# Kernel optimization log

Hardware: AMD Instinct MI355X
Metric: run time of the kernel (lower is better)

Reference implementation:

```python
import jax, jax.numpy as jnp
import numpy as np

ANCHOR_SIZE = np.array([[32.64, 47.68], [50.24, 108.16], [126.72, 96.32], [78.4, 201.92], [178.24, 178.56], [129.6, 294.72], [331.84, 194.56], [227.84, 325.76], [365.44, 358.72]], dtype=np.float32).reshape(3, 3, 2)
STRIDES = [8, 16, 32]
INPUT_SIZE = 640
A = 3            # anchors per level
C = 80           # num_classes
CONF_T = 0.3
NMS_T = 0.5
TOPK = 1000      # fixed candidate budget for jit-compatible greedy NMS
CLS_OFFSET = 4.0 # boxes are in [0,1]; offsetting by class id makes cross-class IoU ~0


def _make_grids():
    gs, ss, aw = [], [], []
    for i, s in enumerate(STRIDES):
        hs = ws = INPUT_SIZE // s
        yy, xx = np.meshgrid(np.arange(hs), np.arange(ws), indexing='ij')
        gs.append(np.stack([xx, yy], -1).reshape(hs * ws, 1, 2).astype(np.float32))
        ss.append(np.full((hs * ws, A, 2), s, np.float32))
        aw.append(np.tile(ANCHOR_SIZE[i][None], (hs * ws, 1, 1)))
    return (jnp.asarray(np.concatenate(gs, 0)),   # [HW, 1, 2]
            jnp.asarray(np.concatenate(ss, 0)),   # [HW, A, 2]
            jnp.asarray(np.concatenate(aw, 0)))   # [HW, A, 2]

GRID, STRIDE_T, ANCH_WH = _make_grids()


def _conv(x, w, b, pad):
    y = jax.lax.conv_general_dilated(x, w, (1, 1), pad, dimension_numbers=('NCHW', 'OIHW', 'NCHW'))
    return y + b[None, :, None, None]


def _conv_bn_lrelu(x, w, b, g, be, m, v):
    y = _conv(x, w, b, 'SAME')
    y = (y - m[None, :, None, None]) * (g / jnp.sqrt(v + 1e-5))[None, :, None, None] + be[None, :, None, None]
    return jnp.where(y > 0, y, 0.1 * y)  # LeakyReLU(0.1)


def _split_head(pred):
    # pred: [B, A*(1+C+4), H, W] -> conf [B,HW*A,1], cls [B,HW*A,C], txt [B,HW,A,4]
    B, ch, H, W = pred.shape
    p = pred.transpose(0, 2, 3, 1).reshape(B, H * W, ch)
    conf = p[:, :, :A].reshape(B, H * W * A, 1)
    cls = p[:, :, A:(1 + C) * A].reshape(B, H * W * A, C)
    txt = p[:, :, (1 + C) * A:].reshape(B, H * W, A, 4)
    return conf, cls, txt


def _nms_single(boxes, sc, cls):
    # boxes [N,4] in [0,1], sc [N], cls [N] -> keep mask [N]
    N = boxes.shape[0]
    masked = jnp.where(sc >= CONF_T, sc, -1.0)
    vals, idx = jax.lax.top_k(masked, TOPK)           # sorted desc, like argsort()[::-1]
    valid = vals >= CONF_T
    b = boxes[idx] + cls[idx].astype(boxes.dtype)[:, None] * CLS_OFFSET
    x1, y1, x2, y2 = b[:, 0], b[:, 1], b[:, 2], b[:, 3]
    area = (x2 - x1) * (y2 - y1)
    xx1 = jnp.maximum(x1[:, None], x1[None, :])
    yy1 = jnp.maximum(y1[:, None], y1[None, :])
    xx2 = jnp.minimum(x2[:, None], x2[None, :])
    yy2 = jnp.minimum(y2[:, None], y2[None, :])
    inter = jnp.maximum(1e-28, xx2 - xx1) * jnp.maximum(1e-28, yy2 - yy1)
    iou = inter / (area[:, None] + area[None, :] - inter)
    sup = iou > NMS_T
    rng = jnp.arange(TOPK)

    def body(i, keep):
        suppressed = jnp.any(keep & sup[:, i] & (rng < i))
        return keep.at[i].set(valid[i] & ~suppressed)

    keep_c = jax.lax.fori_loop(0, TOPK, body, jnp.zeros(TOPK, dtype=bool))
    return jnp.zeros(N, dtype=bool).at[idx].set(keep_c)


def _forward_dense(p3, p4, p5, w1, b1, g1, be1, m1, v1, pw1, pb1, w2, b2, g2, be2, m2, v2, pw2, pb2, w3, b3, g3, be3, m3, v3, pw3, pb3):
    pred_1 = _conv(_conv_bn_lrelu(p3, w1, b1, g1, be1, m1, v1), pw1, pb1, 'VALID')
    pred_2 = _conv(_conv_bn_lrelu(p4, w2, b2, g2, be2, m2, v2), pw2, pb2, 'VALID')
    pred_3 = _conv(_conv_bn_lrelu(p5, w3, b3, g3, be3, m3, v3), pw3, pb3, 'VALID')
    confs, clss, txts = zip(*[_split_head(p) for p in (pred_1, pred_2, pred_3)])
    conf = jnp.concatenate(confs, 1)   # [B, N, 1]
    cls = jnp.concatenate(clss, 1)     # [B, N, C]
    txt = jnp.concatenate(txts, 1)     # [B, HW, A, 4]
    B = txt.shape[0]
    # decode_boxes
    cxy = (jax.nn.sigmoid(txt[..., :2]) + GRID[None]) * STRIDE_T[None]
    wh = jnp.exp(txt[..., 2:]) * ANCH_WH[None]
    xywh = jnp.concatenate([cxy, wh], -1).reshape(B, -1, 4)
    x1y1 = xywh[..., :2] - xywh[..., 2:] / 2
    x2y2 = xywh[..., :2] + xywh[..., 2:] / 2
    boxes = jnp.clip(jnp.concatenate([x1y1, x2y2], -1) / INPUT_SIZE, 0.0, 1.0)  # [B,N,4]
    scores = jax.nn.softmax(cls, axis=-1) * jax.nn.sigmoid(conf)                 # [B,N,C]
    cls_inds = jnp.argmax(scores, axis=-1)                                        # [B,N]
    sc = jnp.max(scores, axis=-1)                                                 # [B,N]
    cx = (boxes[..., 0] + boxes[..., 2]) / 2 * INPUT_SIZE
    cy = (boxes[..., 1] + boxes[..., 3]) / 2 * INPUT_SIZE
    bw = (boxes[..., 2] - boxes[..., 0]) * INPUT_SIZE
    bh = (boxes[..., 3] - boxes[..., 1]) * INPUT_SIZE
    dets5 = jnp.stack([cx, cy, bw, bh, sc], -1)  # [B,N,5]
    return dets5, boxes, sc, cls_inds


def setup_inputs() -> dict:
    key = jax.random.key(0)
    ks = iter(jax.random.split(key, 64))
    d = {
        'p3': jax.random.normal(next(ks), (8, 128, 80, 80), jnp.float32),
        'p4': jax.random.normal(next(ks), (8, 256, 40, 40), jnp.float32),
        'p5': jax.random.normal(next(ks), (8, 512, 20, 20), jnp.float32),
    }
    for lvl, (cin, cout) in zip('123', [(128, 256), (256, 512), (512, 1024)]):
        fan = cin * 9
        d['w' + lvl] = jax.random.normal(next(ks), (cout, cin, 3, 3), jnp.float32) * fan ** -0.5
        d['b' + lvl] = jax.random.normal(next(ks), (cout,), jnp.float32) * 0.1
        d['g' + lvl] = jax.random.uniform(next(ks), (cout,), jnp.float32) * 0.5 + 0.75
        d['be' + lvl] = jax.random.normal(next(ks), (cout,), jnp.float32) * 0.1
        d['m' + lvl] = jax.random.normal(next(ks), (cout,), jnp.float32) * 0.1
        d['v' + lvl] = jax.random.uniform(next(ks), (cout,), jnp.float32) * 0.5 + 0.5
        abC = A * (1 + 4 + C)
        d['pw' + lvl] = jax.random.normal(next(ks), (abC, cout, 1, 1), jnp.float32) * cout ** -0.5
        d['pb' + lvl] = jax.random.normal(next(ks), (abC,), jnp.float32) * 0.1
    return d


def reference(p3, p4, p5, w1, b1, g1, be1, m1, v1, pw1, pb1, w2, b2, g2, be2, m2, v2, pw2, pb2, w3, b3, g3, be3, m3, v3, pw3, pb3):
    dets5, boxes, sc, cls_inds = _forward_dense(p3, p4, p5, w1, b1, g1, be1, m1, v1, pw1, pb1, w2, b2, g2, be2, m2, v2, pw2, pb2, w3, b3, g3, be3, m3, v3, pw3, pb3)
    keep = jax.vmap(_nms_single)(boxes, sc, cls_inds)  # [B,N] bool, per-class greedy NMS
    return dets5, cls_inds.astype(jnp.int32), keep
```

## Files before the change

kernel.cpp:

```cpp
#include <hip/hip_runtime.h>
#include <hip/hip_bf16.h>
#include <stdint.h>
#include <math.h>

typedef unsigned long long ull;
typedef __attribute__((ext_vector_type(8))) _Float16 f16x8;
typedef __attribute__((ext_vector_type(4))) float f32x4;

__device__ __forceinline__ void f16_split(float v, short& hi, short& lo) {
  _Float16 h = (_Float16)v;
  float r = v - (float)h;
  _Float16 l = (_Float16)(r * 2048.f);
  hi = __builtin_bit_cast(short, h);
  lo = __builtin_bit_cast(short, l);
}
__device__ __forceinline__ unsigned pk2(short a, short b) {
  return (unsigned)(unsigned short)a | ((unsigned)(unsigned short)b << 16);
}

__global__ __launch_bounds__(256)
void xprep(const float* __restrict__ x, short* __restrict__ XC, int HW, int CIN) {
  __shared__ float T[32 * 132];
  const int p0 = blockIdx.x * 128, c0 = blockIdx.y * 32, b = blockIdx.z;
  const int tid = threadIdx.x;
#pragma unroll
  for (int i = 0; i < 16; ++i) {
    int u = tid + i * 256;
    int ch = u >> 7, px = u & 127;
    int gp = p0 + px;
    float v = 0.f;
    if (gp < HW) v = x[((size_t)b * CIN + c0 + ch) * HW + gp];
    T[ch * 132 + px] = v;
  }
  __syncthreads();
  const int px = tid & 127, half = tid >> 7;
  const int gp = p0 + px;
  if (gp < HW) {
    short h[16], l[16];
#pragma unroll
    for (int k = 0; k < 16; ++k)
      f16_split(T[(half * 16 + k) * 132 + px], h[k], l[k]);
    short* dh = XC + ((size_t)b * HW + gp) * 2 * CIN + c0 + half * 16;
    short* dl = dh + CIN;
    int4 a, bq;
    a.x = pk2(h[0], h[1]); a.y = pk2(h[2], h[3]); a.z = pk2(h[4], h[5]); a.w = pk2(h[6], h[7]);
    bq.x = pk2(h[8], h[9]); bq.y = pk2(h[10], h[11]); bq.z = pk2(h[12], h[13]); bq.w = pk2(h[14], h[15]);
    *(int4*)dh = a; *(int4*)(dh + 8) = bq;
    a.x = pk2(l[0], l[1]); a.y = pk2(l[2], l[3]); a.z = pk2(l[4], l[5]); a.w = pk2(l[6], l[7]);
    bq.x = pk2(l[8], l[9]); bq.y = pk2(l[10], l[11]); bq.z = pk2(l[12], l[13]); bq.w = pk2(l[14], l[15]);
    *(int4*)dl = a; *(int4*)(dl + 8) = bq;
  }
}

__global__ __launch_bounds__(256)
void wprep(const float* __restrict__ w, const float* __restrict__ g,
           const float* __restrict__ v, short* __restrict__ WF, int CIN, int lgNOG) {
  const int NOG = 1 << lgNOG;
  int e = blockIdx.x * 256 + threadIdx.x;
  int lane = e & 63;
  int og = (e >> 6) & (NOG - 1);
  int r = e >> (6 + lgNOG);
  int t = r % 9, kc = r / 9;
  int oc = og * 16 + (lane & 15);
  int icb = kc * 32 + (lane >> 4) * 8;
  float s = g[oc] / sqrtf(v[oc] + 1e-5f);
  short h[8], l[8];
#pragma unroll
  for (int j = 0; j < 8; ++j) {
    float val = w[((size_t)oc * CIN + icb + j) * 9 + t] * s;
    f16_split(val, h[j], l[j]);
  }
  size_t base = ((size_t)(kc * 9 + t) * NOG + og) * 1024 + lane * 8;
  int4 a;
  a.x = pk2(h[0], h[1]); a.y = pk2(h[2], h[3]); a.z = pk2(h[4], h[5]); a.w = pk2(h[6], h[7]);
  *(int4*)&WF[base] = a;
  a.x = pk2(l[0], l[1]); a.y = pk2(l[2], l[3]); a.z = pk2(l[4], l[5]); a.w = pk2(l[6], l[7]);
  *(int4*)&WF[base + 512] = a;
}

__global__ __launch_bounds__(256)
void hwprep(const float* __restrict__ pw, short* __restrict__ WH, int CIN) {
  int e = blockIdx.x * 256 + threadIdx.x;
  int lane = e & 63;
  int og = (e >> 6) & 15;
  int kc = e >> 10;
  int oc = og * 16 + (lane & 15);
  int ic0 = kc * 32 + (lane >> 4) * 8;
  short h[8], l[8];
#pragma unroll
  for (int j = 0; j < 8; ++j) {
    float val = (oc < 255) ? pw[(size_t)oc * CIN + ic0 + j] : 0.f;
    f16_split(val, h[j], l[j]);
  }
  size_t base = ((size_t)(kc * 16 + og) * 2) * 512 + lane * 8;
  int4 a;
  a.x = pk2(h[0], h[1]); a.y = pk2(h[2], h[3]); a.z = pk2(h[4], h[5]); a.w = pk2(h[6], h[7]);
  *(int4*)&WH[base] = a;
  a.x = pk2(l[0], l[1]); a.y = pk2(l[2], l[3]); a.z = pk2(l[4], l[5]); a.w = pk2(l[6], l[7]);
  *(int4*)&WH[base + 512] = a;
}

__global__ __launch_bounds__(256)
void bfold(const float* __restrict__ b, const float* __restrict__ g,
           const float* __restrict__ be, const float* __restrict__ m,
           const float* __restrict__ v, float* __restrict__ bias2, int n) {
  int i = blockIdx.x * 256 + threadIdx.x;
  if (i < n) bias2[i] = (b[i] - m[i]) * (g[i] / sqrtf(v[i] + 1e-5f)) + be[i];
}

template<int CIN, int COUT, int H, int W, int ROWS, int OG>
__global__ __launch_bounds__(256, 2)
void conv3x3_mfma(const short* __restrict__ XC, const short* __restrict__ WF,
                  const float* __restrict__ bias2, short* __restrict__ ACT) {
  constexpr int HW = H * W, WP = W + 2, NROW = ROWS + 2, NOGT = COUT / 16;
  constexpr int BSH = OG * 1024;
  __shared__ short Xs[NROW * WP * 64];
  __shared__ short Bs[2][BSH];
  const int tid = threadIdx.x, lane = tid & 63, wave = tid >> 6;
  const int tile = blockIdx.x, octile = blockIdx.y, b = blockIdx.z;
  const int r0 = tile * ROWS;
  const int tile_px0 = r0 * W;
  const int kgrp = lane >> 4, lm = lane & 15;
  int Pbase[5];
#pragma unroll
  for (int m = 0; m < 5; ++m) {
    int pl = wave * 80 + m * 16 + lm;
    Pbase[m] = (pl / W) * WP + (pl % W);
  }
  f32x4 acc0[5][OG], acc1[5][OG];
#pragma unroll
  for (int m = 0; m < 5; ++m)
#pragma unroll
    for (int og = 0; og < OG; ++og) {
      acc0[m][og] = (f32x4){0.f, 0.f, 0.f, 0.f};
      acc1[m][og] = (f32x4){0.f, 0.f, 0.f, 0.f};
    }

  const size_t xcb = (size_t)b * HW * 2 * CIN;
  const int og0 = octile * OG;

  for (int u = tid; u < NROW * 2 * 8; u += 256) {
    int sub = u & 7, rc = u >> 3;
    int pxi = (rc >> 1) * WP + ((rc & 1) ? (W + 1) : 0);
    *(int4*)&Xs[pxi * 64 + ((sub ^ (pxi & 7)) << 3)] = make_int4(0, 0, 0, 0);
  }

  for (int kc = 0; kc < CIN / 32; ++kc) {
    for (int g0 = tid; g0 < NROW * W * 8; g0 += 256) {
      int sub = g0 & 7, px = g0 >> 3;
      int rr = px / W, col = px % W;
      int gr = r0 - 1 + rr;
      int pxi = rr * WP + col + 1;
      int dst = pxi * 64 + ((sub ^ (pxi & 7)) << 3);
      if (gr >= 0 && gr < H) {
        const short* src = XC + xcb + (size_t)(gr * W + col) * 2 * CIN +
                           ((sub & 4) ? CIN : 0) + kc * 32 + (sub & 3) * 8;
        *(int4*)&Xs[dst] = *(const int4*)src;
      } else {
        *(int4*)&Xs[dst] = make_int4(0, 0, 0, 0);
      }
    }
    {
      const short* src = WF + ((size_t)(kc * 9 + 0) * NOGT + og0) * 1024 + tid * (BSH / 256);
      *(int4*)&Bs[0][tid * (BSH / 256)] = *(const int4*)src;
      if constexpr (OG == 4)
        *(int4*)&Bs[0][tid * 16 + 8] = *(const int4*)(src + 8);
    }
    __syncthreads();
#pragma unroll 1
    for (int t = 0; t < 9; ++t) {
      int4 r0v, r1v;
      if (t < 8) {
        const short* src = WF + ((size_t)(kc * 9 + t + 1) * NOGT + og0) * 1024 + tid * (BSH / 256);
        r0v = *(const int4*)src;
        if constexpr (OG == 4) r1v = *(const int4*)(src + 8);
      }
      const short* bs = Bs[t & 1];
      f16x8 bh[OG], bl[OG];
#pragma unroll
      for (int og = 0; og < OG; ++og) {
        bh[og] = *(const f16x8*)&bs[(og * 2 + 0) * 512 + lane * 8];
        bl[og] = *(const f16x8*)&bs[(og * 2 + 1) * 512 + lane * 8];
      }
      const int tp = (t / 3) * WP + (t % 3);
#pragma unroll
      for (int m = 0; m < 5; ++m) {
        int P = Pbase[m] + tp;
        int base = P * 64, ph = P & 7;
        f16x8 ah = *(const f16x8*)&Xs[base + ((kgrp ^ ph) << 3)];
        f16x8 al = *(const f16x8*)&Xs[base + (((kgrp + 4) ^ ph) << 3)];
#pragma unroll
        for (int og = 0; og < OG; ++og) {
          acc0[m][og] = __builtin_amdgcn_mfma_f32_16x16x32_f16(bh[og], ah, acc0[m][og], 0, 0, 0);
          acc1[m][og] = __builtin_amdgcn_mfma_f32_16x16x32_f16(bl[og], ah, acc1[m][og], 0, 0, 0);
          acc1[m][og] = __builtin_amdgcn_mfma_f32_16x16x32_f16(bh[og], al, acc1[m][og], 0, 0, 0);
        }
      }
      if (t < 8) {
        *(int4*)&Bs[(t + 1) & 1][tid * (BSH / 256)] = r0v;
        if constexpr (OG == 4)
          *(int4*)&Bs[(t + 1) & 1][tid * 16 + 8] = r1v;
      }
      __syncthreads();
    }
  }
#pragma unroll
  for (int og = 0; og < OG; ++og) {
    const int oc0 = octile * OG * 16 + og * 16 + kgrp * 4;
    float4 bv = *(const float4*)&bias2[oc0];
#pragma unroll
    for (int m = 0; m < 5; ++m) {
      int px = tile_px0 + wave * 80 + m * 16 + lm;
      if (px < HW) {
        f32x4 v0 = acc0[m][og], v1 = acc1[m][og];
        float o0 = fmaf(v1[0], 4.8828125e-4f, v0[0]) + bv.x;
        float o1 = fmaf(v1[1], 4.8828125e-4f, v0[1]) + bv.y;
        float o2 = fmaf(v1[2], 4.8828125e-4f, v0[2]) + bv.z;
        float o3 = fmaf(v1[3], 4.8828125e-4f, v0[3]) + bv.w;
        o0 = o0 > 0.f ? o0 : 0.1f * o0;
        o1 = o1 > 0.f ? o1 : 0.1f * o1;
        o2 = o2 > 0.f ? o2 : 0.1f * o2;
        o3 = o3 > 0.f ? o3 : 0.1f * o3;
        short h[4], l[4];
        f16_split(o0, h[0], l[0]); f16_split(o1, h[1], l[1]);
        f16_split(o2, h[2], l[2]); f16_split(o3, h[3], l[3]);
        short* d = ACT + ((size_t)(b * HW + px)) * 2 * COUT + oc0;
        uint2 hv, lv;
        hv.x = pk2(h[0], h[1]); hv.y = pk2(h[2], h[3]);
        lv.x = pk2(l[0], l[1]); lv.y = pk2(l[2], l[3]);
        *(uint2*)d = hv;
        *(uint2*)(d + COUT) = lv;
      }
    }
  }
}

template<int CIN>
__global__ __launch_bounds__(256)
void head_mfma_decode(const short* __restrict__ ACT, const short* __restrict__ WH,
                      const float* __restrict__ pb,
                      int HW, int Wl, float strd, int P0,
                      float aw0, float ah0, float aw1, float ah1, float aw2, float ah2,
                      float* __restrict__ out, float* __restrict__ boxes,
                      float* __restrict__ scb, int* __restrict__ clsb) {
  __shared__ float pred[32 * 256];
  const int tid = threadIdx.x, lane = tid & 63, wave = tid >> 6;
  const int lm = lane & 15, kgrp = lane >> 4;
  const int pt = blockIdx.x, b = blockIdx.y;
  const int p0 = pt * 32;
  const int ogb = wave * 4;
  int pxg[2];
#pragma unroll
  for (int m = 0; m < 2; ++m) pxg[m] = min(p0 + m * 16 + lm, HW - 1);
  const short* actb = ACT + (size_t)b * HW * 2 * CIN;
  f32x4 acc0[2][4], acc1[2][4], acc2[2][4];
#pragma unroll
  for (int m = 0; m < 2; ++m)
#pragma unroll
    for (int og = 0; og < 4; ++og) {
      acc0[m][og] = (f32x4){0.f, 0.f, 0.f, 0.f};
      acc1[m][og] = (f32x4){0.f, 0.f, 0.f, 0.f};
      acc2[m][og] = (f32x4){0.f, 0.f, 0.f, 0.f};
    }
#pragma unroll 2
  for (int kc = 0; kc < CIN / 32; ++kc) {
    f16x8 ah[2], al[2], wh[4], wl[4];
#pragma unroll
    for (int m = 0; m < 2; ++m) {
      const short* s = actb + (size_t)pxg[m] * 2 * CIN + kc * 32 + kgrp * 8;
      ah[m] = *(const f16x8*)s;
      al[m] = *(const f16x8*)(s + CIN);
    }
#pragma unroll
    for (int og = 0; og < 4; ++og) {
      const short* s = WH + ((size_t)(kc * 16 + ogb + og) * 2) * 512 + lane * 8;
      wh[og] = *(const f16x8*)s;
      wl[og] = *(const f16x8*)(s + 512);
    }
#pragma unroll
    for (int m = 0; m < 2; ++m)
#pragma unroll
      for (int og = 0; og < 4; ++og) {
        acc0[m][og] = __builtin_amdgcn_mfma_f32_16x16x32_f16(wh[og], ah[m], acc0[m][og], 0, 0, 0);
        acc1[m][og] = __builtin_amdgcn_mfma_f32_16x16x32_f16(wl[og], ah[m], acc1[m][og], 0, 0, 0);
        acc1[m][og] = __builtin_amdgcn_mfma_f32_16x16x32_f16(wh[og], al[m], acc1[m][og], 0, 0, 0);
        acc2[m][og] = __builtin_amdgcn_mfma_f32_16x16x32_f16(wl[og], al[m], acc2[m][og], 0, 0, 0);
      }
  }
#pragma unroll
  for (int m = 0; m < 2; ++m) {
    const int pxl = m * 16 + lm;
    const int swz = pxl & 28;
#pragma unroll
    for (int og = 0; og < 4; ++og) {
      const int ch0 = (ogb + og) * 16 + kgrp * 4;
      float4 v;
      const float c = 4.8828125e-4f;
#pragma unroll
      for (int j = 0; j < 4; ++j) {
        float pbv = (ch0 + j < 255) ? pb[ch0 + j] : 0.f;
        float t = fmaf(acc2[m][og][j], c, acc1[m][og][j]);
        (&v.x)[j] = fmaf(t, c, acc0[m][og][j]) + pbv;
      }
      *(float4*)&pred[pxl * 256 + (ch0 ^ swz)] = v;
    }
  }
  __syncthreads();
  if (tid < 96) {
    const int px = tid & 31, a = tid >> 5;
    const int p = p0 + px;
    if (p < HW) {
      const int swz = px & 28;
      const float* pr = &pred[px * 256];
#define RD(ch) pr[(ch) ^ swz]
      float conf = RD(a);
      int ch0 = 3 + 80 * a;
      float m = -1e30f; int ci = 0;
      for (int i = 0; i < 80; ++i) {
        float v = RD(ch0 + i);
        if (v > m) { m = v; ci = i; }
      }
      float ssum = 0.f;
      for (int i = 0; i < 80; ++i) ssum += expf(RD(ch0 + i) - m);
      float sig = 1.f / (1.f + expf(-conf));
      float sc = sig / ssum;
      float tx = RD(243 + 4 * a), ty = RD(244 + 4 * a);
      float tw = RD(245 + 4 * a), th = RD(246 + 4 * a);
#undef RD
      float gxx = (float)(p % Wl), gy = (float)(p / Wl);
      float aw = (a == 0) ? aw0 : ((a == 1) ? aw1 : aw2);
      float ah = (a == 0) ? ah0 : ((a == 1) ? ah1 : ah2);
      float cx = (1.f / (1.f + expf(-tx)) + gxx) * strd;
      float cy2 = (1.f / (1.f + expf(-ty)) + gy) * strd;
      float bw = expf(tw) * aw, bh = expf(th) * ah;
      float x1 = fminf(fmaxf((cx - bw * 0.5f) / 640.f, 0.f), 1.f);
      float y1 = fminf(fmaxf((cy2 - bh * 0.5f) / 640.f, 0.f), 1.f);
      float x2 = fminf(fmaxf((cx + bw * 0.5f) / 640.f, 0.f), 1.f);
      float y2 = fminf(fmaxf((cy2 + bh * 0.5f) / 640.f, 0.f), 1.f);
      int n = (P0 + p) * 3 + a;
      size_t gg = (size_t)b * 25200 + n;
      out[gg * 5 + 0] = (x1 + x2) * 0.5f * 640.f;
      out[gg * 5 + 1] = (y1 + y2) * 0.5f * 640.f;
      out[gg * 5 + 2] = (x2 - x1) * 640.f;
      out[gg * 5 + 3] = (y2 - y1) * 640.f;
      out[gg * 5 + 4] = sc;
      out[(size_t)8 * 25200 * 5 + gg] = (float)ci;
      out[(size_t)8 * 25200 * 6 + gg] = 0.f;
      boxes[gg * 4 + 0] = x1; boxes[gg * 4 + 1] = y1;
      boxes[gg * 4 + 2] = x2; boxes[gg * 4 + 3] = y2;
      scb[gg] = sc; clsb[gg] = ci;
    }
  }
}

__global__ __launch_bounds__(256)
void topk_sort(const float* __restrict__ scb, const float* __restrict__ boxes,
               const int* __restrict__ clsb,
               int* __restrict__ tidx, int* __restrict__ tval, float* __restrict__ tbox) {
  __shared__ ull keys[4096];
  __shared__ int cnt;
  const int b = blockIdx.x, tid = threadIdx.x;
  if (tid == 0) cnt = 0;
  __syncthreads();
  for (int n = tid; n < 25200; n += 256) {
    float s = scb[(size_t)b * 25200 + n];
    if (s >= 0.3f) {
      int p = atomicAdd(&cnt, 1);
      if (p < 4096)
        keys[p] = ((ull)__float_as_uint(s) << 32) | (ull)(0xFFFFFFFFu - (unsigned)n);
    }
  }
  __syncthreads();
  int c = min(cnt, 4096);
  int P2 = 1024;
  while (P2 < c) P2 <<= 1;
  for (int i = c + tid; i < P2; i += 256) keys[i] = 0ull;
  __syncthreads();
  for (int len = 2; len <= P2; len <<= 1) {
    for (int j = len >> 1; j > 0; j >>= 1) {
      for (int x = tid; x < P2; x += 256) {
        int y = x ^ j;
        if (y > x) {
          ull a = keys[x], bb = keys[y];
          bool up = (x & len) == 0;
          if (up ? (a < bb) : (a > bb)) { keys[x] = bb; keys[y] = a; }
        }
      }
      __syncthreads();
    }
  }
  for (int i = tid; i < 1000; i += 256) {
    ull k = keys[i];
    int valid = (k != 0ull) ? 1 : 0;
    int n = valid ? (int)(0xFFFFFFFFu - (unsigned)(k & 0xFFFFFFFFull)) : 0;
    float cls = (float)clsb[(size_t)b * 25200 + n];
    float off = cls * 4.0f;
    const float* bp = &boxes[((size_t)b * 25200 + n) * 4];
    tidx[b * 1000 + i] = n;
    tval[b * 1000 + i] = valid;
    tbox[(b * 1000 + i) * 4 + 0] = bp[0] + off;
    tbox[(b * 1000 + i) * 4 + 1] = bp[1] + off;
    tbox[(b * 1000 + i) * 4 + 2] = bp[2] + off;
    tbox[(b * 1000 + i) * 4 + 3] = bp[3] + off;
  }
}

__global__ __launch_bounds__(1024)
void supmask(const float* __restrict__ tbox, ull* __restrict__ sup) {
  __shared__ float4 bj[64];
  __shared__ float arj[64];
  const int jc = blockIdx.x, b = blockIdx.y;
  const int tid = threadIdx.x;
  if (tid < 64) {
    int j = min(jc * 64 + tid, 999);
    float4 v = *(const float4*)&tbox[((size_t)b * 1000 + j) * 4];
    bj[tid] = v;
    arj[tid] = (v.z - v.x) * (v.w - v.y);
  }
  __syncthreads();
  if (tid < 1000) {
    float4 bi = *(const float4*)&tbox[((size_t)b * 1000 + tid) * 4];
    float ai = (bi.z - bi.x) * (bi.w - bi.y);
    ull w = 0;
#pragma unroll 8
    for (int j = 0; j < 64; ++j) {
      float4 bv = bj[j];
      float xx1 = fmaxf(bi.x, bv.x), yy1 = fmaxf(bi.y, bv.y);
      float xx2 = fminf(bi.z, bv.z), yy2 = fminf(bi.w, bv.w);
      float inter = fmaxf(1e-28f, xx2 - xx1) * fmaxf(1e-28f, yy2 - yy1);
      float iou = inter / (ai + arj[j] - inter);
      if (iou > 0.5f) w |= 1ull << j;
    }
    sup[((size_t)b * 1000 + tid) * 16 + jc] = w;
  }
}

__global__ __launch_bounds__(64)
void nms_kernel(const ull* __restrict__ sup, const int* __restrict__ tval,
                const int* __restrict__ tidx, float* __restrict__ keep_out) {
  const int b = blockIdx.x, lane = threadIdx.x;
  __shared__ ull slds[64][17];
  ull keepw = 0;
  for (int ch = 0; ch < 16; ++ch) {
    int i0 = ch * 64;
    int nIn = min(64, 1000 - i0);
    for (int k = 0; k < 16; ++k) {
      int linear = k * 64 + lane;
      int row = linear >> 4, w = linear & 15;
      slds[row][w] = (row < nIn) ? sup[((size_t)b * 1000 + i0 + row) * 16 + w] : 0ull;
    }
    int myvalid = (lane < nIn) ? tval[b * 1000 + i0 + lane] : 0;
    int myidx = (lane < nIn) ? tidx[b * 1000 + i0 + lane] : 0;
    __syncthreads();
    for (int li = 0; li < nIn; ++li) {
      ull m = (lane < 16) ? (keepw & slds[li][lane]) : 0ull;
      bool sup_any = __any(m != 0ull);
      int v = __shfl(myvalid, li);
      bool keep_i = v && !sup_any;
      if (keep_i) {
        if (lane == ch) keepw |= 1ull << li;
        if (lane == li) keep_out[(size_t)b * 25200 + myidx] = 1.0f;
      }
    }
    __syncthreads();
  }
}

extern "C" void kernel_launch(void* const* d_in, const int* in_sizes, int n_in,
                              void* d_out, int out_size, void* d_ws, size_t ws_size,
                              hipStream_t stream) {
  const float* p3 = (const float*)d_in[0];
  const float* p4 = (const float*)d_in[1];
  const float* p5 = (const float*)d_in[2];
  auto L = [&](int lvl, int k) { return (const float*)d_in[3 + lvl * 8 + k]; };
  float* out = (float*)d_out;
  char* ws = (char*)d_ws;
  size_t o = 0;
  short* ACT = (short*)(ws + o);   o += (size_t)26214400 * 2;
  short* XC  = (short*)(ws + o);   o += (size_t)13107200 * 2;
  short* WF  = (short*)(ws + o);   o += (size_t)9437184 * 2;
  float* bias2 = (float*)(ws + o); o += 2048 * 4;
  float* boxes = (float*)(ws + o); o += (size_t)806400 * 4;
  float* scb = (float*)(ws + o);   o += (size_t)201600 * 4;
  int* clsb = (int*)(ws + o);      o += (size_t)201600 * 4;
  int* tidx = (int*)(ws + o);      o += 8000 * 4;
  int* tval = (int*)(ws + o);      o += 8000 * 4;
  float* tbox = (float*)(ws + o);  o += 32000 * 4;
  ull* sup = (ull*)(ws + o);       o += (size_t)128000 * 8;
  short* WH = XC + (13107200 - 524288);
  float* b2_1 = bias2, *b2_2 = bias2 + 256, *b2_3 = bias2 + 768;

  bfold<<<1, 256, 0, stream>>>(L(0, 1), L(0, 2), L(0, 3), L(0, 4), L(0, 5), b2_1, 256);
  bfold<<<2, 256, 0, stream>>>(L(1, 1), L(1, 2), L(1, 3), L(1, 4), L(1, 5), b2_2, 512);
  bfold<<<4, 256, 0, stream>>>(L(2, 1), L(2, 2), L(2, 3), L(2, 4), L(2, 5), b2_3, 1024);

  wprep<<<144, 256, 0, stream>>>(L(0, 0), L(0, 2), L(0, 5), WF, 128, 4);
  xprep<<<dim3(50, 4, 8), 256, 0, stream>>>(p3, XC, 6400, 128);
  conv3x3_mfma<128, 256, 80, 80, 4, 4><<<dim3(20, 4, 8), 256, 0, stream>>>(XC, WF, b2_1, ACT);
  hwprep<<<32, 256, 0, stream>>>(L(0, 6), WH, 256);
  head_mfma_decode<256><<<dim3(200, 8), 256, 0, stream>>>(
      ACT, WH, L(0, 7), 6400, 80, 8.f, 0,
      32.64f, 47.68f, 50.24f, 108.16f, 126.72f, 96.32f, out, boxes, scb, clsb);
  wprep<<<576, 256, 0, stream>>>(L(1, 0), L(1, 2), L(1, 5), WF, 256, 5);
  xprep<<<dim3(13, 8, 8), 256, 0, stream>>>(p4, XC, 1600, 256);
  conv3x3_mfma<256, 512, 40, 40, 8, 4><<<dim3(5, 8, 8), 256, 0, stream>>>(XC, WF, b2_2, ACT);
  hwprep<<<64, 256, 0, stream>>>(L(1, 6), WH, 512);
  head_mfma_decode<512><<<dim3(50, 8), 256, 0, stream>>>(
      ACT, WH, L(1, 7), 1600, 40, 16.f, 6400,
      78.4f, 201.92f, 178.24f, 178.56f, 129.6f, 294.72f, out, boxes, scb, clsb);
  wprep<<<2304, 256, 0, stream>>>(L(2, 0), L(2, 2), L(2, 5), WF, 512, 6);
  xprep<<<dim3(4, 16, 8), 256, 0, stream>>>(p5, XC, 400, 512);
  conv3x3_mfma<512, 1024, 20, 20, 16, 2><<<dim3(2, 32, 8), 256, 0, stream>>>(XC, WF, b2_3, ACT);
  hwprep<<<128, 256, 0, stream>>>(L(2, 6), WH, 1024);
  head_mfma_decode<1024><<<dim3(13, 8), 256, 0, stream>>>(
      ACT, WH, L(2, 7), 400, 20, 32.f, 8000,
      331.84f, 194.56f, 227.84f, 325.76f, 365.44f, 358.72f, out, boxes, scb, clsb);
  topk_sort<<<8, 256, 0, stream>>>(scb, boxes, clsb, tidx, tval, tbox);
  supmask<<<dim3(16, 8), 1024, 0, stream>>>(tbox, sup);
  nms_kernel<<<8, 64, 0, stream>>>(sup, tval, tidx, out + (size_t)8 * 25200 * 6);
}
```

Before: 0.9996 ms.

## Rewrite greedy NMS to iterate only over kept boxes using removed bitmasks

The NMS kernel no longer walks every candidate with a wave-wide any-vote against a keep mask staged in LDS. It keeps a per-lane 'removed' bitmask and, within each 64-box chunk, jumps straight to the next surviving valid box with ffs. Each kept box ORs its suppression row into the mask. This drops the LDS staging and __syncthreads and skips suppressed boxes entirely, at the cost of serial dependent global loads per kept box.

```diff
diff --git a/kernel.cpp b/kernel.cpp
--- a/kernel.cpp
+++ b/kernel.cpp
@@ -439,30 +439,24 @@
 void nms_kernel(const ull* __restrict__ sup, const int* __restrict__ tval,
                 const int* __restrict__ tidx, float* __restrict__ keep_out) {
   const int b = blockIdx.x, lane = threadIdx.x;
-  __shared__ ull slds[64][17];
-  ull keepw = 0;
-  for (int ch = 0; ch < 16; ++ch) {
-    int i0 = ch * 64;
-    int nIn = min(64, 1000 - i0);
-    for (int k = 0; k < 16; ++k) {
-      int linear = k * 64 + lane;
-      int row = linear >> 4, w = linear & 15;
-      slds[row][w] = (row < nIn) ? sup[((size_t)b * 1000 + i0 + row) * 16 + w] : 0ull;
-    }
+  const ull* supb = sup + (size_t)b * 16000;
+  ull removed = 0;
+  for (int c = 0; c < 16; ++c) {
+    const int i0 = c * 64;
+    const int nIn = min(64, 1000 - i0);
     int myvalid = (lane < nIn) ? tval[b * 1000 + i0 + lane] : 0;
     int myidx = (lane < nIn) ? tidx[b * 1000 + i0 + lane] : 0;
-    __syncthreads();
-    for (int li = 0; li < nIn; ++li) {
-      ull m = (lane < 16) ? (keepw & slds[li][lane]) : 0ull;
-      bool sup_any = __any(m != 0ull);
-      int v = __shfl(myvalid, li);
-      bool keep_i = v && !sup_any;
-      if (keep_i) {
-        if (lane == ch) keepw |= 1ull << li;
-        if (lane == li) keep_out[(size_t)b * 25200 + myidx] = 1.0f;
-      }
-    }
-    __syncthreads();
+    ull w = __ballot(myvalid != 0) & ~__shfl(removed, c);
+    while (w) {
+      int il = __ffsll((long long)w) - 1;
+      int i = i0 + il;
+      ull row_l = (lane < 16) ? supb[(size_t)i * 16 + lane] : 0ull;
+      ull row_c = supb[(size_t)i * 16 + c];
+      if (lane == il) keep_out[(size_t)b * 25200 + myidx] = 1.0f;
+      removed |= row_l;
+      w &= ~row_c;
+      w &= ~(1ull << il);
+    }
   }
 }
 
```

After: 861.3 us. 13.8% less time.
